# Kernel tuning notes

Hardware: AMD Instinct MI355X
Metric: run time of the kernel (lower is better)

## Reference

```python
import jax, jax.numpy as jnp
import numpy as np

N = 100000      # nodes
E = 1600000     # edges (avg degree 16)
IN = 128        # in_channels
HID = 128       # hidden_channels
OUT = 2         # out_channels
NEG_SLOPE = 0.2  # PyG GATConv default


def setup_inputs() -> dict:
    key = jax.random.key(0)
    ks = jax.random.split(key, 20)
    inp = {
        "x": jax.random.normal(ks[0], (N, IN), dtype=jnp.float32),
        "edge_index": jax.random.randint(ks[1], (2, E), 0, N, dtype=jnp.int32),
    }
    # GATConv params (heads=1): W:[din,dout], attention vecs a_src/a_dst:[dout], bias:[dout]
    dims = [(IN, HID), (HID, HID), (HID, HID)]
    for i, (din, dout) in enumerate(dims, start=1):
        base = 4 * i
        inp[f"W{i}"] = jax.random.normal(ks[base], (din, dout), dtype=jnp.float32) * (1.0 / np.sqrt(din))
        inp[f"a{i}s"] = jax.random.normal(ks[base + 1], (dout,), dtype=jnp.float32) * 0.1
        inp[f"a{i}d"] = jax.random.normal(ks[base + 2], (dout,), dtype=jnp.float32) * 0.1
        inp[f"b{i}"] = jnp.zeros((dout,), dtype=jnp.float32)
    inp["Wc"] = jax.random.normal(ks[16], (HID, OUT), dtype=jnp.float32) * (1.0 / np.sqrt(HID))
    inp["bc"] = jnp.zeros((OUT,), dtype=jnp.float32)
    return inp


def _gat_layer(x, src, dst, W, a_s, a_d, b, n):
    # Linear transform: [n, dout]
    h = x @ W
    # Edge attention logits: alpha_src[j] + alpha_dst[i], LeakyReLU (PyG GATConv)
    e = jax.nn.leaky_relu(jnp.take(h @ a_s, src) + jnp.take(h @ a_d, dst), NEG_SLOPE)
    # Stable softmax over incoming edges per destination node
    m = jax.ops.segment_max(e, dst, num_segments=n)
    ex = jnp.exp(e - m[dst])
    denom = jax.ops.segment_sum(ex, dst, num_segments=n)
    alpha = ex / denom[dst]
    # Weighted scatter-aggregation of source features into destinations
    out = jax.ops.segment_sum(alpha[:, None] * jnp.take(h, src, axis=0), dst, num_segments=n)
    return out + b


def reference(x, edge_index, W1, a1s, a1d, b1, W2, a2s, a2d, b2, W3, a3s, a3d, b3, Wc, bc):
    n = x.shape[0]
    # PyG GATConv default add_self_loops=True
    loop = jnp.arange(n, dtype=edge_index.dtype)
    src = jnp.concatenate([edge_index[0], loop])
    dst = jnp.concatenate([edge_index[1], loop])
    for (W, a_s, a_d, b) in ((W1, a1s, a1d, b1), (W2, a2s, a2d, b2), (W3, a3s, a3d, b3)):
        x = jax.nn.relu(_gat_layer(x, src, dst, W, a_s, a_d, b, n))
    return x @ Wc + bc
```

## Files before the change

kernel.cpp:

```cpp
#include <hip/hip_runtime.h>
#include <hip/hip_fp16.h>

#define NNODES 100000
#define NEDGES 1600000
#define DIM 128
#define NB ((NNODES + 63) / 64)
#define NCH 128
#define CHUNK ((NEDGES + NCH - 1) / NCH)
#define EBUF 2560

__device__ __forceinline__ float leaky02(float t) { return t > 0.f ? t : 0.2f * t; }

union H8u { uint2 u; __half2 h[2]; };

__global__ __launch_bounds__(256) void gemm_dots(const float* __restrict__ X,
                                                 const float* __restrict__ W,
                                                 const float* __restrict__ as_,
                                                 const float* __restrict__ ad_,
                                                 __half* __restrict__ H,
                                                 float* __restrict__ s,
                                                 float* __restrict__ d, int n) {
    __shared__ float xs[64][129];
    int t = threadIdx.x;
    int brow = blockIdx.x * 64;
    for (int i = t; i < 64 * 32; i += 256) {
        int r = i >> 5, c4 = (i & 31) * 4;
        int gr = brow + r;
        float4 v = (gr < n) ? *(const float4*)(X + (size_t)gr * 128 + c4)
                            : make_float4(0.f, 0.f, 0.f, 0.f);
        xs[r][c4] = v.x; xs[r][c4 + 1] = v.y; xs[r][c4 + 2] = v.z; xs[r][c4 + 3] = v.w;
    }
    __syncthreads();
    int r0 = (t >> 5) * 8;
    int c0 = (t & 31) * 4;
    float acc[8][4] = {};
#pragma unroll 2
    for (int k = 0; k < 128; ++k) {
        float4 wv = *(const float4*)(W + k * 128 + c0);
#pragma unroll
        for (int r = 0; r < 8; ++r) {
            float xr = xs[r0 + r][k];
            acc[r][0] += xr * wv.x;
            acc[r][1] += xr * wv.y;
            acc[r][2] += xr * wv.z;
            acc[r][3] += xr * wv.w;
        }
    }
    float as0 = as_[c0], as1 = as_[c0 + 1], as2 = as_[c0 + 2], as3 = as_[c0 + 3];
    float ad0 = ad_[c0], ad1 = ad_[c0 + 1], ad2 = ad_[c0 + 2], ad3 = ad_[c0 + 3];
    float sp[8], dp[8];
#pragma unroll
    for (int r = 0; r < 8; ++r) {
        int gr = brow + r0 + r;
        if (gr < n) {
            H8u pk;
            pk.h[0] = __floats2half2_rn(acc[r][0], acc[r][1]);
            pk.h[1] = __floats2half2_rn(acc[r][2], acc[r][3]);
            *(uint2*)(H + (size_t)gr * 128 + c0) = pk.u;
        }
        sp[r] = acc[r][0] * as0 + acc[r][1] * as1 + acc[r][2] * as2 + acc[r][3] * as3;
        dp[r] = acc[r][0] * ad0 + acc[r][1] * ad1 + acc[r][2] * ad2 + acc[r][3] * ad3;
    }
#pragma unroll
    for (int off = 16; off; off >>= 1)
#pragma unroll
        for (int r = 0; r < 8; ++r) {
            sp[r] += __shfl_xor(sp[r], off);
            dp[r] += __shfl_xor(dp[r], off);
        }
    if ((t & 31) == 0)
#pragma unroll
        for (int r = 0; r < 8; ++r) {
            int gr = brow + r0 + r;
            if (gr < n) { s[gr] = sp[r]; d[gr] = dp[r]; }
        }
}

__global__ __launch_bounds__(512) void bucket_count(const int* __restrict__ dst,
                                                    int* __restrict__ blockcounts) {
    __shared__ int hist[NB];
    int b = blockIdx.x, t = threadIdx.x;
    for (int i = t; i < NB; i += 512) hist[i] = 0;
    __syncthreads();
    int e0 = b * CHUNK, e1 = min(NEDGES, e0 + CHUNK);
    for (int e = e0 + t; e < e1; e += 512)
        atomicAdd(&hist[dst[e] >> 6], 1);
    __syncthreads();
    for (int i = t; i < NB; i += 512)
        blockcounts[i * NCH + b] = hist[i];
}

__global__ __launch_bounds__(NCH) void bucket_scan_a(int* __restrict__ blockcounts,
                                                     int* __restrict__ btotal) {
    int bin = blockIdx.x, t = threadIdx.x;
    int v = blockcounts[bin * NCH + t];
    int incl = v;
#pragma unroll
    for (int off = 1; off < 64; off <<= 1) {
        int u = __shfl_up(incl, off, 64);
        if ((t & 63) >= off) incl += u;
    }
    __shared__ int wsum;
    if (t == 63) wsum = incl;
    __syncthreads();
    int excl = incl - v + ((t >= 64) ? wsum : 0);
    blockcounts[bin * NCH + t] = excl;
    if (t == NCH - 1) btotal[bin] = excl + v;
}

__global__ __launch_bounds__(1024) void bucket_scan_b(const int* __restrict__ btotal,
                                                      int* __restrict__ bbase) {
    __shared__ int ts[2][1024];
    int t = threadIdx.x;
    int b0 = t * 2;
    int c0 = (b0 < NB)     ? btotal[b0]     : 0;
    int c1 = (b0 + 1 < NB) ? btotal[b0 + 1] : 0;
    int sum = c0 + c1;
    ts[0][t] = sum;
    __syncthreads();
    int sb = 0;
    for (int off = 1; off < 1024; off <<= 1) {
        int v = ts[sb][t] + ((t >= off) ? ts[sb][t - off] : 0);
        ts[sb ^ 1][t] = v;
        sb ^= 1;
        __syncthreads();
    }
    int excl = ts[sb][t] - sum;
    if (b0 < NB)     bbase[b0]     = excl;
    if (b0 + 1 < NB) bbase[b0 + 1] = excl + c0;
    if (t == 1023) bbase[NB] = ts[sb][1023];
}

__global__ __launch_bounds__(512) void bucket_scatter(const int* __restrict__ src,
                                                      const int* __restrict__ dst,
                                                      const int* __restrict__ blockcounts,
                                                      const int* __restrict__ bbase,
                                                      int* __restrict__ packed) {
    __shared__ int cur[NB];
    int b = blockIdx.x, t = threadIdx.x;
    for (int i = t; i < NB; i += 512) cur[i] = bbase[i] + blockcounts[i * NCH + b];
    __syncthreads();
    int e0 = b * CHUNK, e1 = min(NEDGES, e0 + CHUNK);
    for (int e = e0 + t; e < e1; e += 512) {
        int dv = dst[e];
        int bin = dv >> 6;
        int p = atomicAdd(&cur[bin], 1);
        packed[p] = ((dv & 63) << 17) | src[e];
    }
}

__global__ __launch_bounds__(256) void bucket_csr(const int* __restrict__ packed,
                                                  const int* __restrict__ bbase,
                                                  int* __restrict__ rowptr,
                                                  int* __restrict__ csr_src) {
    __shared__ int ebuf[EBUF];
    __shared__ int hist[64], cur[64];
    int i = blockIdx.x, t = threadIdx.x;
    int base = bbase[i], cnt = bbase[i + 1] - base;
    bool inl = (cnt <= EBUF);
    if (inl) for (int j = t; j < cnt; j += 256) ebuf[j] = packed[base + j];
    if (t < 64) hist[t] = 0;
    __syncthreads();
    for (int j = t; j < cnt; j += 256) {
        int v = inl ? ebuf[j] : packed[base + j];
        atomicAdd(&hist[v >> 17], 1);
    }
    __syncthreads();
    if (t < 64) {
        int h = hist[t];
        int incl = h;
#pragma unroll
        for (int off = 1; off < 64; off <<= 1) {
            int u = __shfl_up(incl, off, 64);
            if (t >= off) incl += u;
        }
        int ex = incl - h;
        cur[t] = ex;
        int node = i * 64 + t;
        if (node <= NNODES) rowptr[node] = base + ex;
    }
    __syncthreads();
    for (int j = t; j < cnt; j += 256) {
        int v = inl ? ebuf[j] : packed[base + j];
        int off = atomicAdd(&cur[v >> 17], 1);
        csr_src[base + off] = v & 0x1FFFF;
    }
}

template <bool LAST>
__global__ __launch_bounds__(256) void gat_gather(const int* __restrict__ rowptr,
                                                  const int* __restrict__ csr,
                                                  const float* __restrict__ s,
                                                  const float* __restrict__ d,
                                                  const __half* __restrict__ H,
                                                  const float* __restrict__ bias,
                                                  const float* __restrict__ Wc,
                                                  const float* __restrict__ bc,
                                                  float* __restrict__ A,
                                                  float* __restrict__ out, int n) {
    int node = blockIdx.x * 4 + (threadIdx.x >> 6);
    if (node >= n) return;
    int lane = threadIdx.x & 63;
    int half = lane >> 5;
    int pos  = lane & 31;
    int base = rowptr[node];
    int deg  = rowptr[node + 1] - base;
    float dnode = d[node];
    float snode = s[node];

    float4 acc = make_float4(0.f, 0.f, 0.f, 0.f);
    float denom;

    if (deg < 64) {
        int cnt = deg + 1;
        int si  = (lane < deg) ? csr[base + lane] : node;
        float sv = (lane < deg) ? s[si] : snode;
        float lv = leaky02(sv + dnode);
        float lm = (lane < cnt) ? lv : -1e30f;
#pragma unroll
        for (int off = 32; off; off >>= 1) lm = fmaxf(lm, __shfl_xor(lm, off));
        float w = (lane < cnt) ? expf(lv - lm) : 0.f;
        denom = w;
#pragma unroll
        for (int off = 32; off; off >>= 1) denom += __shfl_xor(denom, off);

        int cnt16 = (cnt + 15) & ~15;
        for (int j = 0; j < cnt16; j += 16) {
            float wk[8]; int sk[8];
#pragma unroll
            for (int k = 0; k < 8; ++k) {
                int ii = j + 2 * k + half;
                wk[k] = __shfl(w, ii);
                sk[k] = __shfl(si, ii);
            }
            H8u hv[8];
#pragma unroll
            for (int k = 0; k < 8; ++k)
                hv[k].u = *(const uint2*)(H + (size_t)sk[k] * 128 + pos * 4);
#pragma unroll
            for (int k = 0; k < 8; ++k) {
                float2 a01 = __half22float2(hv[k].h[0]);
                float2 a23 = __half22float2(hv[k].h[1]);
                acc.x += wk[k] * a01.x;
                acc.y += wk[k] * a01.y;
                acc.z += wk[k] * a23.x;
                acc.w += wk[k] * a23.y;
            }
        }
    } else {
        float m = -1e30f;
        for (int c = 0; c <= deg; c += 64) {
            int idx = c + lane;
            float lv = -1e30f;
            if (idx < deg)       lv = leaky02(s[csr[base + idx]] + dnode);
            else if (idx == deg) lv = leaky02(snode + dnode);
            m = fmaxf(m, lv);
        }
#pragma unroll
        for (int off = 32; off; off >>= 1) m = fmaxf(m, __shfl_xor(m, off));
        denom = 0.f;
        for (int c = 0; c <= deg; c += 64) {
            int idx = c + lane;
            int cnt = min(64, deg + 1 - c);
            int si = (idx < deg) ? csr[base + idx] : node;
            float w = 0.f;
            if (idx < deg)       w = expf(leaky02(s[si] + dnode) - m);
            else if (idx == deg) w = expf(leaky02(snode + dnode) - m);
            denom += w;
            int cnt16 = (cnt + 15) & ~15;
            for (int j = 0; j < cnt16; j += 16) {
                float wk[8]; int sk[8];
#pragma unroll
                for (int k = 0; k < 8; ++k) {
                    int ii = j + 2 * k + half;
                    wk[k] = __shfl(w, ii);
                    sk[k] = __shfl(si, ii);
                }
                H8u hv[8];
#pragma unroll
                for (int k = 0; k < 8; ++k)
                    hv[k].u = *(const uint2*)(H + (size_t)sk[k] * 128 + pos * 4);
#pragma unroll
                for (int k = 0; k < 8; ++k) {
                    float2 a01 = __half22float2(hv[k].h[0]);
                    float2 a23 = __half22float2(hv[k].h[1]);
                    acc.x += wk[k] * a01.x;
                    acc.y += wk[k] * a01.y;
                    acc.z += wk[k] * a23.x;
                    acc.w += wk[k] * a23.y;
                }
            }
        }
#pragma unroll
        for (int off = 32; off; off >>= 1) denom += __shfl_xor(denom, off);
    }

    acc.x += __shfl_xor(acc.x, 32);
    acc.y += __shfl_xor(acc.y, 32);
    acc.z += __shfl_xor(acc.z, 32);
    acc.w += __shfl_xor(acc.w, 32);
    if (half == 0) {
        float inv = 1.f / denom;
        float4 o;
        o.x = fmaxf(acc.x * inv + bias[pos * 4 + 0], 0.f);
        o.y = fmaxf(acc.y * inv + bias[pos * 4 + 1], 0.f);
        o.z = fmaxf(acc.z * inv + bias[pos * 4 + 2], 0.f);
        o.w = fmaxf(acc.w * inv + bias[pos * 4 + 3], 0.f);
        if (!LAST) {
            *(float4*)(A + (size_t)node * 128 + pos * 4) = o;
        } else {
            float c0v = o.x * Wc[(pos * 4 + 0) * 2] + o.y * Wc[(pos * 4 + 1) * 2] +
                        o.z * Wc[(pos * 4 + 2) * 2] + o.w * Wc[(pos * 4 + 3) * 2];
            float c1v = o.x * Wc[(pos * 4 + 0) * 2 + 1] + o.y * Wc[(pos * 4 + 1) * 2 + 1] +
                        o.z * Wc[(pos * 4 + 2) * 2 + 1] + o.w * Wc[(pos * 4 + 3) * 2 + 1];
#pragma unroll
            for (int off = 16; off; off >>= 1) {
                c0v += __shfl_xor(c0v, off);
                c1v += __shfl_xor(c1v, off);
            }
            if (pos == 0) {
                out[(size_t)node * 2 + 0] = c0v + bc[0];
                out[(size_t)node * 2 + 1] = c1v + bc[1];
            }
        }
    }
}

extern "C" void kernel_launch(void* const* d_in, const int* in_sizes, int n_in,
                              void* d_out, int out_size, void* d_ws, size_t ws_size,
                              hipStream_t stream) {
    const float* x   = (const float*)d_in[0];
    const int*   ei  = (const int*)d_in[1];
    const int*   src = ei;
    const int*   dst = ei + NEDGES;
    const float* Ws[3]  = {(const float*)d_in[2], (const float*)d_in[6], (const float*)d_in[10]};
    const float* ass[3] = {(const float*)d_in[3], (const float*)d_in[7], (const float*)d_in[11]};
    const float* ads[3] = {(const float*)d_in[4], (const float*)d_in[8], (const float*)d_in[12]};
    const float* bs[3]  = {(const float*)d_in[5], (const float*)d_in[9], (const float*)d_in[13]};
    const float* Wc = (const float*)d_in[14];
    const float* bc = (const float*)d_in[15];
    float* out = (float*)d_out;

    const int n = NNODES;

    float*  abuf = (float*)d_ws;
    float*  sbuf = abuf + (size_t)n * DIM;
    float*  dbuf = sbuf + n;
    __half* h16  = (__half*)(dbuf + n);
    int*    rowptr      = (int*)(h16 + (size_t)n * DIM);
    int*    csr_src     = rowptr + n + 1;
    int*    packed      = csr_src + NEDGES;
    int*    blockcounts = packed + NEDGES;
    int*    bbase       = blockcounts + NB * NCH;
    int*    btotal      = bbase + NB + 1;

    const int g64         = (n + 63) / 64;
    const int gather_grid = (n + 3) / 4;

    bucket_count<<<NCH, 512, 0, stream>>>(dst, blockcounts);
    bucket_scan_a<<<NB, NCH, 0, stream>>>(blockcounts, btotal);
    bucket_scan_b<<<1, 1024, 0, stream>>>(btotal, bbase);
    bucket_scatter<<<NCH, 512, 0, stream>>>(src, dst, blockcounts, bbase, packed);
    bucket_csr<<<NB, 256, 0, stream>>>(packed, bbase, rowptr, csr_src);

    const float* xin = x;
    for (int layer = 0; layer < 3; ++layer) {
        gemm_dots<<<g64, 256, 0, stream>>>(xin, Ws[layer], ass[layer], ads[layer],
                                           h16, sbuf, dbuf, n);
        if (layer == 2)
            gat_gather<true><<<gather_grid, 256, 0, stream>>>(
                rowptr, csr_src, sbuf, dbuf, h16, bs[layer], Wc, bc, abuf, out, n);
        else
            gat_gather<false><<<gather_grid, 256, 0, stream>>>(
                rowptr, csr_src, sbuf, dbuf, h16, bs[layer], Wc, bc, abuf, out, n);
        xin = abuf;
    }
}
```

Baseline: 440.2 us.

## Use fp16 MFMA for the node GEMM and store intermediate activations in fp16

Replaces the scalar FP32 GEMM with fp16 MFMA 16x16x32 instructions. Inputs and the transposed weight are staged in LDS as half precision. Layer outputs are now written as fp16, which halves activation write and read traffic, and later layers load them directly. The gather's small-degree path now processes leftover edges one pair at a time instead of padding to 16, which avoids wasted loads. The cost is lower precision on inputs and weights, plus 2-byte scattered stores of H in the MFMA epilogue.

```diff
diff --git a/kernel.cpp b/kernel.cpp
--- a/kernel.cpp
+++ b/kernel.cpp
@@ -8,71 +8,109 @@
 #define NCH 128
 #define CHUNK ((NEDGES + NCH - 1) / NCH)
 #define EBUF 2560
+#define LSTR 136
+
+typedef _Float16 f16x8 __attribute__((ext_vector_type(8)));
+typedef float f32x4 __attribute__((ext_vector_type(4)));
 
 __device__ __forceinline__ float leaky02(float t) { return t > 0.f ? t : 0.2f * t; }
 
 union H8u { uint2 u; __half2 h[2]; };
 
-__global__ __launch_bounds__(256) void gemm_dots(const float* __restrict__ X,
+template <bool XF16>
+__global__ __launch_bounds__(256) void gemm_mfma(const float* __restrict__ X,
+                                                 const __half* __restrict__ X16,
                                                  const float* __restrict__ W,
                                                  const float* __restrict__ as_,
                                                  const float* __restrict__ ad_,
                                                  __half* __restrict__ H,
                                                  float* __restrict__ s,
                                                  float* __restrict__ d, int n) {
-    __shared__ float xs[64][129];
+    __shared__ __half As[64][LSTR];
+    __shared__ __half Wt[128][LSTR];
     int t = threadIdx.x;
     int brow = blockIdx.x * 64;
-    for (int i = t; i < 64 * 32; i += 256) {
-        int r = i >> 5, c4 = (i & 31) * 4;
-        int gr = brow + r;
-        float4 v = (gr < n) ? *(const float4*)(X + (size_t)gr * 128 + c4)
-                            : make_float4(0.f, 0.f, 0.f, 0.f);
-        xs[r][c4] = v.x; xs[r][c4 + 1] = v.y; xs[r][c4 + 2] = v.z; xs[r][c4 + 3] = v.w;
-    }
-    __syncthreads();
-    int r0 = (t >> 5) * 8;
-    int c0 = (t & 31) * 4;
-    float acc[8][4] = {};
-#pragma unroll 2
-    for (int k = 0; k < 128; ++k) {
-        float4 wv = *(const float4*)(W + k * 128 + c0);
-#pragma unroll
-        for (int r = 0; r < 8; ++r) {
-            float xr = xs[r0 + r][k];
-            acc[r][0] += xr * wv.x;
-            acc[r][1] += xr * wv.y;
-            acc[r][2] += xr * wv.z;
-            acc[r][3] += xr * wv.w;
-        }
-    }
-    float as0 = as_[c0], as1 = as_[c0 + 1], as2 = as_[c0 + 2], as3 = as_[c0 + 3];
-    float ad0 = ad_[c0], ad1 = ad_[c0 + 1], ad2 = ad_[c0 + 2], ad3 = ad_[c0 + 3];
-    float sp[8], dp[8];
-#pragma unroll
-    for (int r = 0; r < 8; ++r) {
-        int gr = brow + r0 + r;
+
+    if (XF16) {
+        for (int i = t; i < 64 * 16; i += 256) {
+            int r = i >> 4, c8 = (i & 15) * 8;
+            int gr = brow + r;
+            uint4 v = (gr < n) ? *(const uint4*)(X16 + (size_t)gr * 128 + c8)
+                               : make_uint4(0u, 0u, 0u, 0u);
+            *(uint4*)&As[r][c8] = v;
+        }
+    } else {
+        for (int i = t; i < 64 * 32; i += 256) {
+            int r = i >> 5, c4 = (i & 31) * 4;
+            int gr = brow + r;
+            float4 v = (gr < n) ? *(const float4*)(X + (size_t)gr * 128 + c4)
+                                : make_float4(0.f, 0.f, 0.f, 0.f);
+            As[r][c4 + 0] = __float2half_rn(v.x);
+            As[r][c4 + 1] = __float2half_rn(v.y);
+            As[r][c4 + 2] = __float2half_rn(v.z);
+            As[r][c4 + 3] = __float2half_rn(v.w);
+        }
+    }
+    for (int i = t; i < 128 * 32; i += 256) {
+        int k = i >> 5, n4 = (i & 31) * 4;
+        float4 wv = *(const float4*)(W + k * 128 + n4);
+        Wt[n4 + 0][k] = __float2half_rn(wv.x);
+        Wt[n4 + 1][k] = __float2half_rn(wv.y);
+        Wt[n4 + 2][k] = __float2half_rn(wv.z);
+        Wt[n4 + 3][k] = __float2half_rn(wv.w);
+    }
+    __syncthreads();
+
+    int wid  = t >> 6;
+    int lane = t & 63;
+    int lrow = lane & 15;
+    int lkg  = lane >> 4;
+    int r0   = wid * 16;
+
+    f32x4 acc[8] = {};
+#pragma unroll
+    for (int kk = 0; kk < 128; kk += 32) {
+        f16x8 af = *(const f16x8*)&As[r0 + lrow][kk + lkg * 8];
+#pragma unroll
+        for (int ct = 0; ct < 8; ++ct) {
+            f16x8 bf = *(const f16x8*)&Wt[ct * 16 + lrow][kk + lkg * 8];
+            acc[ct] = __builtin_amdgcn_mfma_f32_16x16x32_f16(af, bf, acc[ct], 0, 0, 0);
+        }
+    }
+
+    float sp[4] = {0.f, 0.f, 0.f, 0.f};
+    float dp[4] = {0.f, 0.f, 0.f, 0.f};
+#pragma unroll
+    for (int ct = 0; ct < 8; ++ct) {
+        float a_s = as_[ct * 16 + lrow];
+        float a_d = ad_[ct * 16 + lrow];
+#pragma unroll
+        for (int j = 0; j < 4; ++j) {
+            sp[j] += acc[ct][j] * a_s;
+            dp[j] += acc[ct][j] * a_d;
+        }
+    }
+#pragma unroll
+    for (int j = 0; j < 4; ++j) {
+        int gr = brow + r0 + lkg * 4 + j;
         if (gr < n) {
-            H8u pk;
-            pk.h[0] = __floats2half2_rn(acc[r][0], acc[r][1]);
-            pk.h[1] = __floats2half2_rn(acc[r][2], acc[r][3]);
-            *(uint2*)(H + (size_t)gr * 128 + c0) = pk.u;
-        }
-        sp[r] = acc[r][0] * as0 + acc[r][1] * as1 + acc[r][2] * as2 + acc[r][3] * as3;
-        dp[r] = acc[r][0] * ad0 + acc[r][1] * ad1 + acc[r][2] * ad2 + acc[r][3] * ad3;
-    }
-#pragma unroll
-    for (int off = 16; off; off >>= 1)
-#pragma unroll
-        for (int r = 0; r < 8; ++r) {
-            sp[r] += __shfl_xor(sp[r], off);
-            dp[r] += __shfl_xor(dp[r], off);
-        }
-    if ((t & 31) == 0)
-#pragma unroll
-        for (int r = 0; r < 8; ++r) {
-            int gr = brow + r0 + r;
-            if (gr < n) { s[gr] = sp[r]; d[gr] = dp[r]; }
+#pragma unroll
+            for (int ct = 0; ct < 8; ++ct)
+                H[(size_t)gr * 128 + ct * 16 + lrow] = __float2half_rn(acc[ct][j]);
+        }
+    }
+#pragma unroll
+    for (int off = 1; off < 16; off <<= 1)
+#pragma unroll
+        for (int j = 0; j < 4; ++j) {
+            sp[j] += __shfl_xor(sp[j], off);
+            dp[j] += __shfl_xor(dp[j], off);
+        }
+    if (lrow == 0)
+#pragma unroll
+        for (int j = 0; j < 4; ++j) {
+            int gr = brow + r0 + lkg * 4 + j;
+            if (gr < n) { s[gr] = sp[j]; d[gr] = dp[j]; }
         }
 }
 
@@ -196,7 +234,7 @@
                                                   const float* __restrict__ bias,
                                                   const float* __restrict__ Wc,
                                                   const float* __restrict__ bc,
-                                                  float* __restrict__ A,
+                                                  __half* __restrict__ A16,
                                                   float* __restrict__ out, int n) {
     int node = blockIdx.x * 4 + (threadIdx.x >> 6);
     if (node >= n) return;
@@ -224,8 +262,8 @@
 #pragma unroll
         for (int off = 32; off; off >>= 1) denom += __shfl_xor(denom, off);
 
-        int cnt16 = (cnt + 15) & ~15;
-        for (int j = 0; j < cnt16; j += 16) {
+        int jfull = cnt & ~15;
+        for (int j = 0; j < jfull; j += 16) {
             float wk[8]; int sk[8];
 #pragma unroll
             for (int k = 0; k < 8; ++k) {
@@ -246,6 +284,21 @@
                 acc.z += wk[k] * a23.x;
                 acc.w += wk[k] * a23.y;
             }
+        }
+        int rem = cnt - jfull;
+        int kmax = (rem + 1) >> 1;
+        for (int k = 0; k < kmax; ++k) {
+            int ii = jfull + 2 * k + half;
+            float wv = __shfl(w, ii);
+            int   sv2 = __shfl(si, ii);
+            H8u hv;
+            hv.u = *(const uint2*)(H + (size_t)sv2 * 128 + pos * 4);
+            float2 a01 = __half22float2(hv.h[0]);
+            float2 a23 = __half22float2(hv.h[1]);
+            acc.x += wv * a01.x;
+            acc.y += wv * a01.y;
+            acc.z += wv * a23.x;
+            acc.w += wv * a23.y;
         }
     } else {
         float m = -1e30f;
@@ -307,7 +360,10 @@
         o.z = fmaxf(acc.z * inv + bias[pos * 4 + 2], 0.f);
         o.w = fmaxf(acc.w * inv + bias[pos * 4 + 3], 0.f);
         if (!LAST) {
-            *(float4*)(A + (size_t)node * 128 + pos * 4) = o;
+            H8u pk;
+            pk.h[0] = __floats2half2_rn(o.x, o.y);
+            pk.h[1] = __floats2half2_rn(o.z, o.w);
+            *(uint2*)(A16 + (size_t)node * 128 + pos * 4) = pk.u;
         } else {
             float c0v = o.x * Wc[(pos * 4 + 0) * 2] + o.y * Wc[(pos * 4 + 1) * 2] +
                         o.z * Wc[(pos * 4 + 2) * 2] + o.w * Wc[(pos * 4 + 3) * 2];
@@ -343,11 +399,11 @@
 
     const int n = NNODES;
 
-    float*  abuf = (float*)d_ws;
-    float*  sbuf = abuf + (size_t)n * DIM;
+    __half* h16  = (__half*)d_ws;
+    __half* a16  = h16 + (size_t)n * DIM;
+    float*  sbuf = (float*)(a16 + (size_t)n * DIM);
     float*  dbuf = sbuf + n;
-    __half* h16  = (__half*)(dbuf + n);
-    int*    rowptr      = (int*)(h16 + (size_t)n * DIM);
+    int*    rowptr      = (int*)(dbuf + n);
     int*    csr_src     = rowptr + n + 1;
     int*    packed      = csr_src + NEDGES;
     int*    blockcounts = packed + NEDGES;
@@ -363,16 +419,18 @@
     bucket_scatter<<<NCH, 512, 0, stream>>>(src, dst, blockcounts, bbase, packed);
     bucket_csr<<<NB, 256, 0, stream>>>(packed, bbase, rowptr, csr_src);
 
-    const float* xin = x;
     for (int layer = 0; layer < 3; ++layer) {
-        gemm_dots<<<g64, 256, 0, stream>>>(xin, Ws[layer], ass[layer], ads[layer],
-                                           h16, sbuf, dbuf, n);
+        if (layer == 0)
+            gemm_mfma<false><<<g64, 256, 0, stream>>>(x, a16, Ws[0], ass[0], ads[0],
+                                                      h16, sbuf, dbuf, n);
+        else
+            gemm_mfma<true><<<g64, 256, 0, stream>>>(x, a16, Ws[layer], ass[layer], ads[layer],
+                                                     h16, sbuf, dbuf, n);
         if (layer == 2)
             gat_gather<true><<<gather_grid, 256, 0, stream>>>(
-                rowptr, csr_src, sbuf, dbuf, h16, bs[layer], Wc, bc, abuf, out, n);
+                rowptr, csr_src, sbuf, dbuf, h16, bs[layer], Wc, bc, a16, out, n);
         else
             gat_gather<false><<<gather_grid, 256, 0, stream>>>(
-                rowptr, csr_src, sbuf, dbuf, h16, bs[layer], Wc, bc, abuf, out, n);
-        xin = abuf;
-    }
-}
+                rowptr, csr_src, sbuf, dbuf, h16, bs[layer], Wc, bc, a16, out, n);
+    }
+}
```

Measured after the change: 423.7 us. 3.7% less time.
